# Performance work log

Hardware: AMD Instinct MI355X
Metric: run time of the kernel (lower is better)

Reference implementation:

```python
import jax, jax.numpy as jnp
import numpy as np
import math

B, S, D_MODEL, H = 128, 256, 128, 8
D_K = D_MODEL // H
FACTOR = 5
SAMPLE_K = FACTOR * int(math.ceil(math.log(S)))   # 30 sampled keys per query
N_TOP = min(FACTOR * int(math.ceil(math.log(S))), S)  # 30 active queries
KSIZE = 7


def setup_inputs() -> dict:
    key = jax.random.key(0)
    ks = jax.random.split(key, 10)
    s = 0.05
    return {
        "query": jax.random.normal(ks[0], (B, S, D_MODEL), jnp.float32),
        "key": jax.random.normal(ks[1], (B, S, D_MODEL), jnp.float32),
        "value": jax.random.normal(ks[2], (B, S, D_MODEL), jnp.float32),
        "conv_k_w": jax.random.normal(ks[3], (S, S, KSIZE), jnp.float32) * s,
        "conv_k_b": jax.random.normal(ks[4], (S,), jnp.float32) * s,
        "conv_v_w": jax.random.normal(ks[5], (S, S, KSIZE), jnp.float32) * s,
        "conv_v_b": jax.random.normal(ks[6], (S,), jnp.float32) * s,
        "lin_w": jax.random.normal(ks[7], (D_MODEL, D_MODEL), jnp.float32) * s,
        "lin_b": jax.random.normal(ks[8], (D_MODEL,), jnp.float32) * s,
        "index_sample": jax.random.randint(ks[9], (S, SAMPLE_K), 0, S),
    }


def _rotary(x):
    # x: [B,S,D]; complex rotation of consecutive pairs, angle = pos * theta^{-2i/D}
    half = D_MODEL // 2
    freqs = 1.0 / (10000.0 ** (jnp.arange(0, D_MODEL, 2, dtype=jnp.float32) / D_MODEL))
    ang = jnp.arange(S, dtype=jnp.float32)[:, None] * freqs[None, :]  # [S, half]
    cos, sin = jnp.cos(ang), jnp.sin(ang)
    xr = x.reshape(B, S, half, 2)
    out_r = xr[..., 0] * cos - xr[..., 1] * sin
    out_i = xr[..., 0] * sin + xr[..., 1] * cos
    return jnp.stack([out_r, out_i], axis=-1).reshape(B, S, D_MODEL)


def _causal_conv(x, w, b):
    # x: [B, C=S, L=D_MODEL]; causal => left-pad (KSIZE-1). w: [C_out, C_in, K]
    y = jax.lax.conv_general_dilated(
        x, w, window_strides=(1,), padding=[(KSIZE - 1, 0)],
        dimension_numbers=("NCH", "OIH", "NCH"))
    return y + b[None, :, None]


def reference(query, key, value, conv_k_w, conv_k_b, conv_v_w, conv_v_b,
              lin_w, lin_b, index_sample):
    q, k = _rotary(query), _rotary(key)
    k = _causal_conv(k, conv_k_w, conv_k_b)        # conv over seq-as-channels
    v = _causal_conv(value, conv_v_w, conv_v_b)
    # [B,S,D] -> [B,H,S,Dk]
    q = q.reshape(B, S, H, D_K).transpose(0, 2, 1, 3)
    k = k.reshape(B, S, H, D_K).transpose(0, 2, 1, 3)
    v = v.reshape(B, S, H, D_K).transpose(0, 2, 1, 3)

    # --- ProbSparse attention (Informer), mask=None ---
    k_sample = k[:, :, index_sample, :]                       # [B,H,S,SAMPLE_K,Dk]
    qk_sample = jnp.einsum('bhld,bhlsd->bhls', q, k_sample)   # sampled scores
    M = qk_sample.max(axis=-1) - qk_sample.mean(axis=-1)      # sparsity measure [B,H,S]
    _, m_top = jax.lax.top_k(M, N_TOP)                        # active queries [B,H,u]
    q_reduce = jnp.take_along_axis(q, m_top[..., None], axis=2)  # [B,H,u,Dk]
    scores = jnp.einsum('bhud,bhld->bhul', q_reduce, k) / jnp.sqrt(jnp.float32(D_K))
    attn = jax.nn.softmax(scores, axis=-1)
    out_top = jnp.einsum('bhul,bhld->bhud', attn, v)          # [B,H,u,Dk]
    # initial context = mean of V (no mask); overwrite rows of active queries
    context = jnp.broadcast_to(v.mean(axis=2, keepdims=True), (B, H, S, D_K))
    bi = jnp.arange(B)[:, None, None]
    hi = jnp.arange(H)[None, :, None]
    context = context.at[bi, hi, m_top].set(out_top)

    x = context.transpose(0, 2, 1, 3).reshape(B, S, D_MODEL)
    return x @ lin_w.T + lin_b
```

## Files before the change

### kernel.cpp

```cpp
#include <hip/hip_runtime.h>
#include <math.h>

constexpr int B_  = 128;
constexpr int S_  = 256;
constexpr int D_  = 128;
constexpr int H_  = 8;
constexpr int DK_ = 16;
constexpr int SK_ = 30;
constexpr int NT_ = 30;

typedef short short8  __attribute__((ext_vector_type(8)));
typedef float floatx4 __attribute__((ext_vector_type(4)));

__device__ inline ushort bf16_rne(float f) {
    unsigned u = __float_as_uint(f);
    u += 0x7fffu + ((u >> 16) & 1u);
    return (ushort)(u >> 16);
}
__device__ inline float bf16_to_f(ushort h) {
    return __uint_as_float(((unsigned)h) << 16);
}

__global__ __launch_bounds__(256) void wprep_kernel(
    const float* __restrict__ wk, const float* __restrict__ wv,
    const float* __restrict__ lw,
    ushort* __restrict__ wk_hi, ushort* __restrict__ wk_lo,
    ushort* __restrict__ wv_hi,
    ushort* __restrict__ lw_hi, ushort* __restrict__ lw_lo)
{
    int tid = blockIdx.x * 256 + threadIdx.x;
    if (tid < 131072) {
        int which = tid >> 16;
        int oi = tid & 65535;
        const float* src = (which ? wv : wk) + (size_t)oi * 7;
#pragma unroll
        for (int t = 0; t < 7; t++) {
            float f = src[t];
            ushort hi = bf16_rne(f);
            size_t dst = (size_t)t * 65536 + oi;
            if (which) {
                wv_hi[dst] = hi;
            } else {
                wk_hi[dst] = hi;
                wk_lo[dst] = bf16_rne(f - bf16_to_f(hi));
            }
        }
    } else {
        int ec = tid - 131072;
        float f = lw[ec];
        ushort hi = bf16_rne(f);
        lw_hi[ec] = hi;
        lw_lo[ec] = bf16_rne(f - bf16_to_f(hi));
    }
}

__global__ __launch_bounds__(256) void trig_kernel(float* __restrict__ tab)
{
    int tid = blockIdx.x * 256 + threadIdx.x;
    int f = tid & 63, l = tid >> 6;
    double freq = exp(((double)(-f) / 64.0) * 9.210340371976184);
    double ang  = (double)l * freq;
    tab[tid * 2]     = (float)cos(ang);
    tab[tid * 2 + 1] = (float)sin(ang);
}

__global__ __launch_bounds__(256) void rotary_kernel(
    const float* __restrict__ q, const float* __restrict__ k,
    const float* __restrict__ tab,
    float* __restrict__ q_h, float* __restrict__ k_rot)
{
    int tid = blockIdx.x * 256 + threadIdx.x;
    int f = tid & 63;
    int l = (tid >> 6) & 255;
    int b = tid >> 14;

    float2 cs = *(const float2*)(tab + (size_t)(l * 64 + f) * 2);
    float c = cs.x, s = cs.y;

    int base = (b * S_ + l) * D_ + 2 * f;
    float q0 = q[base], q1 = q[base + 1];
    float k0 = k[base], k1 = k[base + 1];

    float qr = q0 * c - q1 * s;
    float qi = q0 * s + q1 * c;
    float kr = k0 * c - k1 * s;
    float ki = k0 * s + k1 * c;

    k_rot[base]     = kr;
    k_rot[base + 1] = ki;

    int d = 2 * f;
    int h = d >> 4, dk = d & 15;
    int qb = ((b * H_ + h) * S_ + l) * DK_ + dk;
    q_h[qb]     = qr;
    q_h[qb + 1] = qi;
}

__global__ __launch_bounds__(256) void transcvt_kernel(
    const float* __restrict__ k_rot, const float* __restrict__ value,
    ushort* __restrict__ khi_t, ushort* __restrict__ klo_t,
    ushort* __restrict__ vhi_t)
{
    __shared__ float tile[64 * 132];
    int b = blockIdx.x;
    int which = blockIdx.y;
    int tid = threadIdx.x;
    const float* src = which ? value : k_rot;

    for (int lc = 0; lc < 4; lc++) {
        __syncthreads();
        for (int s = tid; s < 2048; s += 256) {
            int l = s >> 5, c4 = s & 31;
            *(float4*)(tile + l * 132 + c4 * 4) =
                *(const float4*)(src + (((size_t)b * 256) + lc * 64 + l) * 128 + c4 * 4);
        }
        __syncthreads();
        int d = tid >> 1, half = tid & 1;
        alignas(16) ushort hh[32], ll[32];
#pragma unroll
        for (int j = 0; j < 32; j++) {
            float f = tile[(half * 32 + j) * 132 + d];
            ushort hb = bf16_rne(f);
            hh[j] = hb;
            ll[j] = bf16_rne(f - bf16_to_f(hb));
        }
        size_t off = (((size_t)b * 128) + d) * 256 + lc * 64 + half * 32;
        if (which) {
#pragma unroll
            for (int m = 0; m < 4; m++) ((uint4*)(vhi_t + off))[m] = ((uint4*)hh)[m];
        } else {
#pragma unroll
            for (int m = 0; m < 4; m++) ((uint4*)(khi_t + off))[m] = ((uint4*)hh)[m];
#pragma unroll
            for (int m = 0; m < 4; m++) ((uint4*)(klo_t + off))[m] = ((uint4*)ll)[m];
        }
    }
}

__global__ __launch_bounds__(256, 4) void conv3_kernel(
    const ushort* __restrict__ khi_t, const ushort* __restrict__ klo_t,
    const ushort* __restrict__ vhi_t,
    const ushort* __restrict__ wk_hi, const ushort* __restrict__ wk_lo,
    const ushort* __restrict__ wv_hi,
    const float* __restrict__ kbias, const float* __restrict__ vbias,
    float* __restrict__ k_h, float* __restrict__ v_h)
{
    constexpr int LI = 72;
    __shared__ ushort xhi[134 * LI];
    __shared__ ushort xlo[134 * LI];

    const bool kp = (blockIdx.z == 0);
    const ushort* xhi_g = kp ? khi_t : vhi_t;
    const ushort* whi   = kp ? wk_hi : wv_hi;
    const float*  bias  = kp ? kbias : vbias;
    float* yh           = kp ? k_h : v_h;

    int b    = blockIdx.x;
    int oblk = blockIdx.y * 64;
    int tid  = threadIdx.x;
    int lane = tid & 63, wid = tid >> 6;
    int lm = lane & 15, kb = lane >> 4;
    int ow = wid >> 1, dw = wid & 1;
    int obase = oblk + ow * 32;
    int dbase = dw * 64;

    floatx4 acc[8];
#pragma unroll
    for (int i = 0; i < 8; i++) acc[i] = (floatx4){0.f, 0.f, 0.f, 0.f};

    for (int idx = tid; idx < 6 * LI; idx += 256) { xhi[idx] = 0; xlo[idx] = 0; }

    const ushort* abase_h = xhi + (dbase + lm) * LI + kb * 8;
    const ushort* abase_l = xlo + (dbase + lm) * LI + kb * 8;

    for (int ic = 0; ic < 4; ic++) {
        __syncthreads();
        for (int s = tid; s < 1024; s += 256) {
            int d = s >> 3, p = s & 7;
            size_t g = (((size_t)b * 128) + d) * 256 + ic * 64 + p * 8;
            *(short8*)(xhi + (d + 6) * LI + p * 8) = *(const short8*)(xhi_g + g);
            if (kp)
                *(short8*)(xlo + (d + 6) * LI + p * 8) = *(const short8*)(klo_t + g);
        }
        __syncthreads();
#pragma unroll
        for (int ks2 = 0; ks2 < 2; ks2++) {
            int ibase = ic * 64 + ks2 * 32 + kb * 8;
#pragma unroll
            for (int t = 0; t < 7; t++) {
                short8 xh[4], xl[4];
#pragma unroll
                for (int nd = 0; nd < 4; nd++) {
                    xh[nd] = *(const short8*)(abase_h + (nd * 16 + t) * LI + ks2 * 32);
                    if (kp) xl[nd] = *(const short8*)(abase_l + (nd * 16 + t) * LI + ks2 * 32);
                }
                short8 wh[2], wl[2];
#pragma unroll
                for (int po = 0; po < 2; po++) {
                    size_t woff = (size_t)t * 65536 + (size_t)(obase + po * 16 + lm) * 256 + ibase;
                    wh[po] = *(const short8*)(whi + woff);
                    if (kp) wl[po] = *(const short8*)(wk_lo + woff);
                }
#pragma unroll
                for (int po = 0; po < 2; po++) {
#pragma unroll
                    for (int nd = 0; nd < 4; nd++) {
                        int a = po * 4 + nd;
                        acc[a] = __builtin_amdgcn_mfma_f32_16x16x32_bf16(xh[nd], wh[po], acc[a], 0, 0, 0);
                        if (kp) {
                            acc[a] = __builtin_amdgcn_mfma_f32_16x16x32_bf16(xl[nd], wh[po], acc[a], 0, 0, 0);
                            acc[a] = __builtin_amdgcn_mfma_f32_16x16x32_bf16(xh[nd], wl[po], acc[a], 0, 0, 0);
                        }
                    }
                }
            }
        }
    }

#pragma unroll
    for (int po = 0; po < 2; po++) {
        int o = obase + po * 16 + lm;
        float bv = bias[o];
#pragma unroll
        for (int nd = 0; nd < 4; nd++) {
            int dhi = dw * 4 + nd;
#pragma unroll
            for (int r = 0; r < 4; r++) {
                int dk = kb * 4 + r;
                yh[(((size_t)b * 8 + dhi) * 256 + o) * 16 + dk] = acc[po * 4 + nd][r] + bv;
            }
        }
    }
}

__global__ __launch_bounds__(256) void topk_kernel(
    const float* __restrict__ q_h, const float* __restrict__ k_h,
    const int* __restrict__ idxs, int* __restrict__ sel)
{
    __shared__ float ks[S_ * 20];
    __shared__ float Marr[S_];
    __shared__ int cnt;
    int bh  = blockIdx.x;
    int tid = threadIdx.x;
    if (tid == 0) cnt = 0;

    const float* kp = k_h + (size_t)bh * S_ * DK_;
    for (int idx = tid; idx < S_ * DK_; idx += 256)
        ks[(idx >> 4) * 20 + (idx & 15)] = kp[idx];
    __syncthreads();

    float qr[16];
    const float4* qp = (const float4*)(q_h + ((size_t)bh * S_ + tid) * DK_);
#pragma unroll
    for (int i = 0; i < 4; i++) {
        float4 t4 = qp[i];
        qr[4*i] = t4.x; qr[4*i+1] = t4.y; qr[4*i+2] = t4.z; qr[4*i+3] = t4.w;
    }
    int idxr[SK_];
    const int* ip = idxs + tid * SK_;
#pragma unroll
    for (int s = 0; s < SK_; s++) idxr[s] = ip[s];

    float mx = -1e30f, sm = 0.f;
#pragma unroll
    for (int s = 0; s < SK_; s++) {
        const float4* kr = (const float4*)(ks + idxr[s] * 20);
        float4 k0 = kr[0], k1 = kr[1], k2 = kr[2], k3 = kr[3];
        float d0 = qr[0]*k0.x, d1 = qr[1]*k0.y, d2 = qr[2]*k0.z, d3 = qr[3]*k0.w;
        d0 = fmaf(qr[4],  k1.x, d0); d1 = fmaf(qr[5],  k1.y, d1);
        d2 = fmaf(qr[6],  k1.z, d2); d3 = fmaf(qr[7],  k1.w, d3);
        d0 = fmaf(qr[8],  k2.x, d0); d1 = fmaf(qr[9],  k2.y, d1);
        d2 = fmaf(qr[10], k2.z, d2); d3 = fmaf(qr[11], k2.w, d3);
        d0 = fmaf(qr[12], k3.x, d0); d1 = fmaf(qr[13], k3.y, d1);
        d2 = fmaf(qr[14], k3.z, d2); d3 = fmaf(qr[15], k3.w, d3);
        float dot = (d0 + d1) + (d2 + d3);
        mx = fmaxf(mx, dot);
        sm += dot;
    }
    float M = mx - sm * (1.0f / 30.0f);
    Marr[tid] = M;
    __syncthreads();

    int higher = 0;
    for (int j = 0; j < S_; j++) {
        float Mj = Marr[j];
        if (Mj > M || (Mj == M && j < tid)) higher++;
    }
    if (higher < NT_) {
        int slot = atomicAdd(&cnt, 1);
        sel[bh * NT_ + slot] = tid;
    }
}

__global__ __launch_bounds__(256) void attn_kernel(
    const float* __restrict__ q_h, const float* __restrict__ k_h,
    const float* __restrict__ v_h, const int* __restrict__ sel,
    ushort* __restrict__ ctx_hi, ushort* __restrict__ ctx_lo)
{
    __shared__ float ks[S_ * 20];
    __shared__ float vs[S_ * 20];
    __shared__ float P[NT_][S_ + 1];
    __shared__ float qs[NT_][16];
    __shared__ float partial[16][17];
    __shared__ float vmean_s[16];
    __shared__ int sel_s[NT_];
    __shared__ int selflag[S_];

    int bh = blockIdx.x, b = bh >> 3, h = bh & 7;
    int tid = threadIdx.x;

    const float* kp = k_h + (size_t)bh * S_ * DK_;
    const float* vp = v_h + (size_t)bh * S_ * DK_;
    for (int idx = tid; idx < S_ * DK_; idx += 256) {
        int r = idx >> 4, c = idx & 15;
        ks[r * 20 + c] = kp[idx];
        vs[r * 20 + c] = vp[idx];
    }
    selflag[tid] = 0;
    if (tid < NT_) sel_s[tid] = sel[bh * NT_ + tid];
    __syncthreads();
    if (tid < NT_) selflag[sel_s[tid]] = 1;
    for (int idx = tid; idx < NT_ * 16; idx += 256) {
        int u = idx >> 4, c = idx & 15;
        qs[u][c] = q_h[((size_t)bh * S_ + sel_s[u]) * DK_ + c];
    }
    {
        int dk = tid & 15, chunk = tid >> 4;
        float s = 0.f;
#pragma unroll
        for (int r = 0; r < 16; r++) s += vs[(chunk * 16 + r) * 20 + dk];
        partial[chunk][dk] = s;
    }
    __syncthreads();
    if (tid < 16) {
        float s = 0.f;
#pragma unroll
        for (int c = 0; c < 16; c++) s += partial[c][tid];
        vmean_s[tid] = s * (1.0f / 256.0f);
    }
    __syncthreads();

    if (!selflag[tid]) {
        alignas(16) ushort hh[16], ll[16];
#pragma unroll
        for (int i = 0; i < 16; i++) {
            float v = vmean_s[i];
            ushort hb = bf16_rne(v);
            hh[i] = hb;
            ll[i] = bf16_rne(v - bf16_to_f(hb));
        }
        size_t off = ((size_t)(b * S_ + tid)) * D_ + h * DK_;
        ((uint4*)(ctx_hi + off))[0] = ((uint4*)hh)[0];
        ((uint4*)(ctx_hi + off))[1] = ((uint4*)hh)[1];
        ((uint4*)(ctx_lo + off))[0] = ((uint4*)ll)[0];
        ((uint4*)(ctx_lo + off))[1] = ((uint4*)ll)[1];
    }

    int g = tid >> 3, j = tid & 7;
    if (g < NT_) {
        float qreg[16];
        const float4* q4 = (const float4*)qs[g];
#pragma unroll
        for (int i = 0; i < 4; i++) {
            float4 t4 = q4[i];
            qreg[4*i] = t4.x; qreg[4*i+1] = t4.y; qreg[4*i+2] = t4.z; qreg[4*i+3] = t4.w;
        }
        float sc[32];
        float mx = -1e30f;
#pragma unroll
        for (int li = 0; li < 32; li++) {
            int l = j + li * 8;
            const float4* kr = (const float4*)(ks + l * 20);
            float4 k0 = kr[0], k1 = kr[1], k2 = kr[2], k3 = kr[3];
            float d0 = qreg[0]*k0.x, d1 = qreg[1]*k0.y, d2 = qreg[2]*k0.z, d3 = qreg[3]*k0.w;
            d0 = fmaf(qreg[4],  k1.x, d0); d1 = fmaf(qreg[5],  k1.y, d1);
            d2 = fmaf(qreg[6],  k1.z, d2); d3 = fmaf(qreg[7],  k1.w, d3);
            d0 = fmaf(qreg[8],  k2.x, d0); d1 = fmaf(qreg[9],  k2.y, d1);
            d2 = fmaf(qreg[10], k2.z, d2); d3 = fmaf(qreg[11], k2.w, d3);
            d0 = fmaf(qreg[12], k3.x, d0); d1 = fmaf(qreg[13], k3.y, d1);
            d2 = fmaf(qreg[14], k3.z, d2); d3 = fmaf(qreg[15], k3.w, d3);
            sc[li] = ((d0 + d1) + (d2 + d3)) * 0.25f;
            mx = fmaxf(mx, sc[li]);
        }
        mx = fmaxf(mx, __shfl_xor(mx, 1));
        mx = fmaxf(mx, __shfl_xor(mx, 2));
        mx = fmaxf(mx, __shfl_xor(mx, 4));
        float se = 0.f;
#pragma unroll
        for (int li = 0; li < 32; li++) {
            float e = __expf(sc[li] - mx);
            P[g][j + li * 8] = e;
            se += e;
        }
        se += __shfl_xor(se, 1);
        se += __shfl_xor(se, 2);
        se += __shfl_xor(se, 4);
        float inv = 1.0f / se;

        int dk0 = j * 2;
        float o0 = 0.f, o1 = 0.f;
#pragma unroll 8
        for (int l = 0; l < S_; l++) {
            float p = P[g][l];
            float2 vv = *(const float2*)(vs + l * 20 + dk0);
            o0 = fmaf(p, vv.x, o0);
            o1 = fmaf(p, vv.y, o1);
        }
        int lrow = sel_s[g];
        float v0 = o0 * inv, v1 = o1 * inv;
        ushort h0 = bf16_rne(v0), h1 = bf16_rne(v1);
        ushort l0 = bf16_rne(v0 - bf16_to_f(h0));
        ushort l1 = bf16_rne(v1 - bf16_to_f(h1));
        size_t off = ((size_t)(b * S_ + lrow)) * D_ + h * DK_ + dk0;
        *(uint*)(ctx_hi + off) = (uint)h0 | ((uint)h1 << 16);
        *(uint*)(ctx_lo + off) = (uint)l0 | ((uint)l1 << 16);
    }
}

__global__ __launch_bounds__(256) void linear_mfma_kernel(
    const ushort* __restrict__ ctx_hi, const ushort* __restrict__ ctx_lo,
    const ushort* __restrict__ w_hi, const ushort* __restrict__ w_lo,
    const float* __restrict__ bias, float* __restrict__ out)
{
    __shared__ ushort ahi[128 * 136];
    __shared__ ushort alo[128 * 136];

    int tid  = threadIdx.x;
    int lane = tid & 63, wid = tid >> 6;
    int lm = lane & 15, kb = lane >> 4;
    size_t rowbase = (size_t)blockIdx.x * 128;

    for (int idx = tid; idx < 2048; idx += 256) {
        int row = idx >> 4, c16 = idx & 15;
        short8 vh = *(const short8*)(ctx_hi + (rowbase + row) * 128 + c16 * 8);
        short8 vl = *(const short8*)(ctx_lo + (rowbase + row) * 128 + c16 * 8);
        *(short8*)(ahi + row * 136 + c16 * 8) = vh;
        *(short8*)(alo + row * 136 + c16 * 8) = vl;
    }
    __syncthreads();

    floatx4 acc[16];
#pragma unroll
    for (int i = 0; i < 16; i++) acc[i] = (floatx4){0.f, 0.f, 0.f, 0.f};

    const ushort* arow_h = ahi + (wid * 32 + lm) * 136 + kb * 8;
    const ushort* arow_l = alo + (wid * 32 + lm) * 136 + kb * 8;

#pragma unroll
    for (int kstep = 0; kstep < 4; kstep++) {
        short8 afh[2], afl[2];
#pragma unroll
        for (int mf = 0; mf < 2; mf++) {
            afh[mf] = *(const short8*)(arow_h + mf * 16 * 136 + kstep * 32);
            afl[mf] = *(const short8*)(arow_l + mf * 16 * 136 + kstep * 32);
        }
        short8 bfh[8], bfl[8];
#pragma unroll
        for (int nf = 0; nf < 8; nf++) {
            bfh[nf] = *(const short8*)(w_hi + (size_t)(nf * 16 + lm) * 128 + kstep * 32 + kb * 8);
            bfl[nf] = *(const short8*)(w_lo + (size_t)(nf * 16 + lm) * 128 + kstep * 32 + kb * 8);
        }
#pragma unroll
        for (int mf = 0; mf < 2; mf++) {
#pragma unroll
            for (int nf = 0; nf < 8; nf++) {
                int a = mf * 8 + nf;
                acc[a] = __builtin_amdgcn_mfma_f32_16x16x32_bf16(afh[mf], bfh[nf], acc[a], 0, 0, 0);
                acc[a] = __builtin_amdgcn_mfma_f32_16x16x32_bf16(afl[mf], bfh[nf], acc[a], 0, 0, 0);
                acc[a] = __builtin_amdgcn_mfma_f32_16x16x32_bf16(afh[mf], bfl[nf], acc[a], 0, 0, 0);
            }
        }
    }

#pragma unroll
    for (int nf = 0; nf < 8; nf++) {
        int col = nf * 16 + lm;
        float bv = bias[col];
#pragma unroll
        for (int mf = 0; mf < 2; mf++) {
#pragma unroll
            for (int r = 0; r < 4; r++) {
                int row = wid * 32 + mf * 16 + kb * 4 + r;
                out[(rowbase + row) * 128 + col] = acc[mf * 8 + nf][r] + bv;
            }
        }
    }
}

extern "C" void kernel_launch(void* const* d_in, const int* in_sizes, int n_in,
                              void* d_out, int out_size, void* d_ws, size_t ws_size,
                              hipStream_t stream)
{
    const float* query = (const float*)d_in[0];
    const float* key   = (const float*)d_in[1];
    const float* value = (const float*)d_in[2];
    const float* ckw   = (const float*)d_in[3];
    const float* ckb   = (const float*)d_in[4];
    const float* cvw   = (const float*)d_in[5];
    const float* cvb   = (const float*)d_in[6];
    const float* lw    = (const float*)d_in[7];
    const float* lb    = (const float*)d_in[8];
    const int*   isamp = (const int*)d_in[9];
    float* out = (float*)d_out;
    float* ws  = (float*)d_ws;

    const size_t NBSD = (size_t)B_ * S_ * D_;
    float* q_h  = ws;
    float* kbuf = ws + NBSD;
    float* k_h  = ws + 2 * NBSD;
    float* v_h  = ws + 3 * NBSD;
    int*   sel  = (int*)(ws + 4 * NBSD);
    ushort* wk_hi = (ushort*)(sel + B_ * H_ * NT_);
    ushort* wk_lo = wk_hi + 7 * 65536;
    ushort* wv_hi = wk_lo + 7 * 65536;
    ushort* lw_hi = wv_hi + 7 * 65536;
    ushort* lw_lo = lw_hi + 16384;
    float*  trig  = (float*)(lw_lo + 16384);
    ushort* khi_t = (ushort*)(trig + 32768);
    ushort* klo_t = khi_t + NBSD;
    ushort* vhi_t = klo_t + NBSD;
    ushort* ctx_hi = (ushort*)kbuf;
    ushort* ctx_lo = ctx_hi + NBSD;

    wprep_kernel<<<dim3(576), 256, 0, stream>>>(ckw, cvw, lw, wk_hi, wk_lo, wv_hi, lw_hi, lw_lo);
    trig_kernel<<<dim3(64), 256, 0, stream>>>(trig);
    rotary_kernel<<<dim3((B_ * S_ * 64) / 256), 256, 0, stream>>>(query, key, trig, q_h, kbuf);
    transcvt_kernel<<<dim3(B_, 2), 256, 0, stream>>>(kbuf, value, khi_t, klo_t, vhi_t);
    conv3_kernel<<<dim3(B_, 4, 2), 256, 0, stream>>>(khi_t, klo_t, vhi_t,
                                                     wk_hi, wk_lo, wv_hi,
                                                     ckb, cvb, k_h, v_h);
    topk_kernel<<<dim3(B_ * H_), 256, 0, stream>>>(q_h, k_h, isamp, sel);
    attn_kernel<<<dim3(B_ * H_), 256, 0, stream>>>(q_h, k_h, v_h, sel, ctx_hi, ctx_lo);
    linear_mfma_kernel<<<dim3(256), 256, 0, stream>>>(ctx_hi, ctx_lo, lw_hi, lw_lo, lb, out);
}
```

Baseline: 284.5 us.

## Fuse trig, rotary, transpose-convert and topk+attention kernels; retile conv warps

Trig-table generation moves into the weight-prep kernel. Rotary, bf16 split and transpose are merged into one kernel so the rotated key is no longer round-tripped through global memory. Top-k selection and attention become one kernel, which removes the sel buffer and a second load of K. The probability matrix in shared memory is replaced by register broadcast via shuffles. The conv warp tiling changes from a 2x2 split to four output-row tiles per warp over 32 d-columns, trading fewer A-operand reads for more weight loads.

```diff
diff --git a/kernel.cpp b/kernel.cpp
--- a/kernel.cpp
+++ b/kernel.cpp
@@ -26,7 +26,8 @@
     const float* __restrict__ lw,
     ushort* __restrict__ wk_hi, ushort* __restrict__ wk_lo,
     ushort* __restrict__ wv_hi,
-    ushort* __restrict__ lw_hi, ushort* __restrict__ lw_lo)
+    ushort* __restrict__ lw_hi, ushort* __restrict__ lw_lo,
+    float* __restrict__ trig)
 {
     int tid = blockIdx.x * 256 + threadIdx.x;
     if (tid < 131072) {
@@ -45,76 +46,61 @@
                 wk_lo[dst] = bf16_rne(f - bf16_to_f(hi));
             }
         }
-    } else {
+    } else if (tid < 147456) {
         int ec = tid - 131072;
         float f = lw[ec];
         ushort hi = bf16_rne(f);
         lw_hi[ec] = hi;
         lw_lo[ec] = bf16_rne(f - bf16_to_f(hi));
-    }
-}
-
-__global__ __launch_bounds__(256) void trig_kernel(float* __restrict__ tab)
-{
-    int tid = blockIdx.x * 256 + threadIdx.x;
-    int f = tid & 63, l = tid >> 6;
-    double freq = exp(((double)(-f) / 64.0) * 9.210340371976184);
-    double ang  = (double)l * freq;
-    tab[tid * 2]     = (float)cos(ang);
-    tab[tid * 2 + 1] = (float)sin(ang);
-}
-
-__global__ __launch_bounds__(256) void rotary_kernel(
+    } else {
+        int t2 = tid - 147456;
+        int f = t2 & 63, l = t2 >> 6;
+        double freq = exp(((double)(-f) / 64.0) * 9.210340371976184);
+        double ang  = (double)l * freq;
+        trig[t2 * 2]     = (float)cos(ang);
+        trig[t2 * 2 + 1] = (float)sin(ang);
+    }
+}
+
+__global__ __launch_bounds__(256) void rotcvt_kernel(
     const float* __restrict__ q, const float* __restrict__ k,
-    const float* __restrict__ tab,
-    float* __restrict__ q_h, float* __restrict__ k_rot)
-{
-    int tid = blockIdx.x * 256 + threadIdx.x;
-    int f = tid & 63;
-    int l = (tid >> 6) & 255;
-    int b = tid >> 14;
-
-    float2 cs = *(const float2*)(tab + (size_t)(l * 64 + f) * 2);
-    float c = cs.x, s = cs.y;
-
-    int base = (b * S_ + l) * D_ + 2 * f;
-    float q0 = q[base], q1 = q[base + 1];
-    float k0 = k[base], k1 = k[base + 1];
-
-    float qr = q0 * c - q1 * s;
-    float qi = q0 * s + q1 * c;
-    float kr = k0 * c - k1 * s;
-    float ki = k0 * s + k1 * c;
-
-    k_rot[base]     = kr;
-    k_rot[base + 1] = ki;
-
-    int d = 2 * f;
-    int h = d >> 4, dk = d & 15;
-    int qb = ((b * H_ + h) * S_ + l) * DK_ + dk;
-    q_h[qb]     = qr;
-    q_h[qb + 1] = qi;
-}
-
-__global__ __launch_bounds__(256) void transcvt_kernel(
-    const float* __restrict__ k_rot, const float* __restrict__ value,
+    const float* __restrict__ value, const float* __restrict__ trig,
+    float* __restrict__ q_h,
     ushort* __restrict__ khi_t, ushort* __restrict__ klo_t,
     ushort* __restrict__ vhi_t)
 {
     __shared__ float tile[64 * 132];
-    int b = blockIdx.x;
-    int which = blockIdx.y;
+    int b  = blockIdx.x;
+    int lc = blockIdx.y;
     int tid = threadIdx.x;
-    const float* src = which ? value : k_rot;
-
-    for (int lc = 0; lc < 4; lc++) {
-        __syncthreads();
-        for (int s = tid; s < 2048; s += 256) {
-            int l = s >> 5, c4 = s & 31;
-            *(float4*)(tile + l * 132 + c4 * 4) =
-                *(const float4*)(src + (((size_t)b * 256) + lc * 64 + l) * 128 + c4 * 4);
-        }
-        __syncthreads();
+
+    for (int s = tid; s < 2048; s += 256) {
+        int l = s >> 5, c4 = s & 31;
+        int lg = lc * 64 + l;
+        float4 qv = *(const float4*)(q + (((size_t)b * 256) + lg) * 128 + c4 * 4);
+        float4 tg = *(const float4*)(trig + ((size_t)lg * 64 + 2 * c4) * 2);
+        float r0 = qv.x * tg.x - qv.y * tg.y;
+        float i0 = qv.x * tg.y + qv.y * tg.x;
+        float r1 = qv.z * tg.z - qv.w * tg.w;
+        float i1 = qv.z * tg.w + qv.w * tg.z;
+        int h = c4 >> 2, dk = (c4 & 3) * 4;
+        *(float4*)(q_h + (((size_t)b * 8 + h) * 256 + lg) * 16 + dk) =
+            make_float4(r0, i0, r1, i1);
+    }
+
+    for (int s = tid; s < 2048; s += 256) {
+        int l = s >> 5, c4 = s & 31;
+        int lg = lc * 64 + l;
+        float4 kv = *(const float4*)(k + (((size_t)b * 256) + lg) * 128 + c4 * 4);
+        float4 tg = *(const float4*)(trig + ((size_t)lg * 64 + 2 * c4) * 2);
+        float r0 = kv.x * tg.x - kv.y * tg.y;
+        float i0 = kv.x * tg.y + kv.y * tg.x;
+        float r1 = kv.z * tg.z - kv.w * tg.w;
+        float i1 = kv.z * tg.w + kv.w * tg.z;
+        *(float4*)(tile + l * 132 + c4 * 4) = make_float4(r0, i0, r1, i1);
+    }
+    __syncthreads();
+    {
         int d = tid >> 1, half = tid & 1;
         alignas(16) ushort hh[32], ll[32];
 #pragma unroll
@@ -125,19 +111,32 @@
             ll[j] = bf16_rne(f - bf16_to_f(hb));
         }
         size_t off = (((size_t)b * 128) + d) * 256 + lc * 64 + half * 32;
-        if (which) {
-#pragma unroll
-            for (int m = 0; m < 4; m++) ((uint4*)(vhi_t + off))[m] = ((uint4*)hh)[m];
-        } else {
-#pragma unroll
-            for (int m = 0; m < 4; m++) ((uint4*)(khi_t + off))[m] = ((uint4*)hh)[m];
-#pragma unroll
-            for (int m = 0; m < 4; m++) ((uint4*)(klo_t + off))[m] = ((uint4*)ll)[m];
-        }
-    }
-}
-
-__global__ __launch_bounds__(256, 4) void conv3_kernel(
+#pragma unroll
+        for (int m = 0; m < 4; m++) ((uint4*)(khi_t + off))[m] = ((uint4*)hh)[m];
+#pragma unroll
+        for (int m = 0; m < 4; m++) ((uint4*)(klo_t + off))[m] = ((uint4*)ll)[m];
+    }
+    __syncthreads();
+
+    for (int s = tid; s < 2048; s += 256) {
+        int l = s >> 5, c4 = s & 31;
+        *(float4*)(tile + l * 132 + c4 * 4) =
+            *(const float4*)(value + (((size_t)b * 256) + lc * 64 + l) * 128 + c4 * 4);
+    }
+    __syncthreads();
+    {
+        int d = tid >> 1, half = tid & 1;
+        alignas(16) ushort hh[32];
+#pragma unroll
+        for (int j = 0; j < 32; j++)
+            hh[j] = bf16_rne(tile[(half * 32 + j) * 132 + d]);
+        size_t off = (((size_t)b * 128) + d) * 256 + lc * 64 + half * 32;
+#pragma unroll
+        for (int m = 0; m < 4; m++) ((uint4*)(vhi_t + off))[m] = ((uint4*)hh)[m];
+    }
+}
+
+__global__ __launch_bounds__(256, 4) void conv4_kernel(
     const ushort* __restrict__ khi_t, const ushort* __restrict__ klo_t,
     const ushort* __restrict__ vhi_t,
     const ushort* __restrict__ wk_hi, const ushort* __restrict__ wk_lo,
@@ -155,14 +154,12 @@
     const float*  bias  = kp ? kbias : vbias;
     float* yh           = kp ? k_h : v_h;
 
-    int b    = blockIdx.x;
-    int oblk = blockIdx.y * 64;
-    int tid  = threadIdx.x;
-    int lane = tid & 63, wid = tid >> 6;
+    int b     = blockIdx.x;
+    int obase = blockIdx.y * 64;
+    int tid   = threadIdx.x;
+    int lane  = tid & 63, dw = tid >> 6;
     int lm = lane & 15, kb = lane >> 4;
-    int ow = wid >> 1, dw = wid & 1;
-    int obase = oblk + ow * 32;
-    int dbase = dw * 64;
+    int dbase = dw * 32;
 
     floatx4 acc[8];
 #pragma unroll
@@ -188,24 +185,24 @@
             int ibase = ic * 64 + ks2 * 32 + kb * 8;
 #pragma unroll
             for (int t = 0; t < 7; t++) {
-                short8 xh[4], xl[4];
-#pragma unroll
-                for (int nd = 0; nd < 4; nd++) {
+                short8 xh[2], xl[2];
+#pragma unroll
+                for (int nd = 0; nd < 2; nd++) {
                     xh[nd] = *(const short8*)(abase_h + (nd * 16 + t) * LI + ks2 * 32);
                     if (kp) xl[nd] = *(const short8*)(abase_l + (nd * 16 + t) * LI + ks2 * 32);
                 }
-                short8 wh[2], wl[2];
-#pragma unroll
-                for (int po = 0; po < 2; po++) {
+                short8 wh[4], wl[4];
+#pragma unroll
+                for (int po = 0; po < 4; po++) {
                     size_t woff = (size_t)t * 65536 + (size_t)(obase + po * 16 + lm) * 256 + ibase;
                     wh[po] = *(const short8*)(whi + woff);
                     if (kp) wl[po] = *(const short8*)(wk_lo + woff);
                 }
 #pragma unroll
-                for (int po = 0; po < 2; po++) {
-#pragma unroll
-                    for (int nd = 0; nd < 4; nd++) {
-                        int a = po * 4 + nd;
+                for (int po = 0; po < 4; po++) {
+#pragma unroll
+                    for (int nd = 0; nd < 2; nd++) {
+                        int a = po * 2 + nd;
                         acc[a] = __builtin_amdgcn_mfma_f32_16x16x32_bf16(xh[nd], wh[po], acc[a], 0, 0, 0);
                         if (kp) {
                             acc[a] = __builtin_amdgcn_mfma_f32_16x16x32_bf16(xl[nd], wh[po], acc[a], 0, 0, 0);
@@ -218,36 +215,48 @@
     }
 
 #pragma unroll
-    for (int po = 0; po < 2; po++) {
+    for (int po = 0; po < 4; po++) {
         int o = obase + po * 16 + lm;
         float bv = bias[o];
 #pragma unroll
-        for (int nd = 0; nd < 4; nd++) {
-            int dhi = dw * 4 + nd;
+        for (int nd = 0; nd < 2; nd++) {
+            int dhi = dw * 2 + nd;
 #pragma unroll
             for (int r = 0; r < 4; r++) {
                 int dk = kb * 4 + r;
-                yh[(((size_t)b * 8 + dhi) * 256 + o) * 16 + dk] = acc[po * 4 + nd][r] + bv;
+                yh[(((size_t)b * 8 + dhi) * 256 + o) * 16 + dk] = acc[po * 2 + nd][r] + bv;
             }
         }
     }
 }
 
-__global__ __launch_bounds__(256) void topk_kernel(
+__global__ __launch_bounds__(256) void topk_attn_kernel(
     const float* __restrict__ q_h, const float* __restrict__ k_h,
-    const int* __restrict__ idxs, int* __restrict__ sel)
+    const float* __restrict__ v_h, const int* __restrict__ idxs,
+    ushort* __restrict__ ctx_hi, ushort* __restrict__ ctx_lo)
 {
     __shared__ float ks[S_ * 20];
+    __shared__ float vs[S_ * 20];
     __shared__ float Marr[S_];
+    __shared__ float qs[NT_][16];
+    __shared__ float partial[16][17];
+    __shared__ float vmean_s[16];
+    __shared__ int sel_s[NT_];
+    __shared__ int selflag[S_];
     __shared__ int cnt;
-    int bh  = blockIdx.x;
+
+    int bh = blockIdx.x, b = bh >> 3, h = bh & 7;
     int tid = threadIdx.x;
     if (tid == 0) cnt = 0;
+    selflag[tid] = 0;
 
     const float* kp = k_h + (size_t)bh * S_ * DK_;
-    for (int idx = tid; idx < S_ * DK_; idx += 256)
-        ks[(idx >> 4) * 20 + (idx & 15)] = kp[idx];
-    __syncthreads();
+    const float* vp = v_h + (size_t)bh * S_ * DK_;
+    for (int idx = tid; idx < S_ * DK_; idx += 256) {
+        int r = idx >> 4, c = idx & 15;
+        ks[r * 20 + c] = kp[idx];
+        vs[r * 20 + c] = vp[idx];
+    }
 
     float qr[16];
     const float4* qp = (const float4*)(q_h + ((size_t)bh * S_ + tid) * DK_);
@@ -260,6 +269,7 @@
     const int* ip = idxs + tid * SK_;
 #pragma unroll
     for (int s = 0; s < SK_; s++) idxr[s] = ip[s];
+    __syncthreads();
 
     float mx = -1e30f, sm = 0.f;
 #pragma unroll
@@ -277,66 +287,41 @@
         mx = fmaxf(mx, dot);
         sm += dot;
     }
-    float M = mx - sm * (1.0f / 30.0f);
-    Marr[tid] = M;
-    __syncthreads();
-
-    int higher = 0;
-    for (int j = 0; j < S_; j++) {
-        float Mj = Marr[j];
-        if (Mj > M || (Mj == M && j < tid)) higher++;
-    }
-    if (higher < NT_) {
-        int slot = atomicAdd(&cnt, 1);
-        sel[bh * NT_ + slot] = tid;
-    }
-}
-
-__global__ __launch_bounds__(256) void attn_kernel(
-    const float* __restrict__ q_h, const float* __restrict__ k_h,
-    const float* __restrict__ v_h, const int* __restrict__ sel,
-    ushort* __restrict__ ctx_hi, ushort* __restrict__ ctx_lo)
-{
-    __shared__ float ks[S_ * 20];
-    __shared__ float vs[S_ * 20];
-    __shared__ float P[NT_][S_ + 1];
-    __shared__ float qs[NT_][16];
-    __shared__ float partial[16][17];
-    __shared__ float vmean_s[16];
-    __shared__ int sel_s[NT_];
-    __shared__ int selflag[S_];
-
-    int bh = blockIdx.x, b = bh >> 3, h = bh & 7;
-    int tid = threadIdx.x;
-
-    const float* kp = k_h + (size_t)bh * S_ * DK_;
-    const float* vp = v_h + (size_t)bh * S_ * DK_;
-    for (int idx = tid; idx < S_ * DK_; idx += 256) {
-        int r = idx >> 4, c = idx & 15;
-        ks[r * 20 + c] = kp[idx];
-        vs[r * 20 + c] = vp[idx];
-    }
-    selflag[tid] = 0;
-    if (tid < NT_) sel_s[tid] = sel[bh * NT_ + tid];
-    __syncthreads();
-    if (tid < NT_) selflag[sel_s[tid]] = 1;
+    Marr[tid] = mx - sm * (1.0f / 30.0f);
+
+    {
+        int dk = tid & 15, chunk = tid >> 4;
+        float s = 0.f;
+#pragma unroll
+        for (int r = 0; r < 16; r++) s += vs[(chunk * 16 + r) * 20 + dk];
+        partial[chunk][dk] = s;
+    }
+    __syncthreads();
+
+    if (tid < 16) {
+        float s = 0.f;
+#pragma unroll
+        for (int c = 0; c < 16; c++) s += partial[c][tid];
+        vmean_s[tid] = s * (1.0f / 256.0f);
+    }
+    {
+        float M = Marr[tid];
+        int higher = 0;
+        for (int j = 0; j < S_; j++) {
+            float Mj = Marr[j];
+            if (Mj > M || (Mj == M && j < tid)) higher++;
+        }
+        if (higher < NT_) {
+            int slot = atomicAdd(&cnt, 1);
+            sel_s[slot] = tid;
+            selflag[tid] = 1;
+        }
+    }
+    __syncthreads();
+
     for (int idx = tid; idx < NT_ * 16; idx += 256) {
         int u = idx >> 4, c = idx & 15;
         qs[u][c] = q_h[((size_t)bh * S_ + sel_s[u]) * DK_ + c];
-    }
-    {
-        int dk = tid & 15, chunk = tid >> 4;
-        float s = 0.f;
-#pragma unroll
-        for (int r = 0; r < 16; r++) s += vs[(chunk * 16 + r) * 20 + dk];
-        partial[chunk][dk] = s;
-    }
-    __syncthreads();
-    if (tid < 16) {
-        float s = 0.f;
-#pragma unroll
-        for (int c = 0; c < 16; c++) s += partial[c][tid];
-        vmean_s[tid] = s * (1.0f / 256.0f);
     }
     __syncthreads();
 
@@ -365,8 +350,8 @@
             float4 t4 = q4[i];
             qreg[4*i] = t4.x; qreg[4*i+1] = t4.y; qreg[4*i+2] = t4.z; qreg[4*i+3] = t4.w;
         }
-        float sc[32];
-        float mx = -1e30f;
+        float e[32];
+        float mxs = -1e30f;
 #pragma unroll
         for (int li = 0; li < 32; li++) {
             int l = j + li * 8;
@@ -379,18 +364,17 @@
             d2 = fmaf(qreg[10], k2.z, d2); d3 = fmaf(qreg[11], k2.w, d3);
             d0 = fmaf(qreg[12], k3.x, d0); d1 = fmaf(qreg[13], k3.y, d1);
             d2 = fmaf(qreg[14], k3.z, d2); d3 = fmaf(qreg[15], k3.w, d3);
-            sc[li] = ((d0 + d1) + (d2 + d3)) * 0.25f;
-            mx = fmaxf(mx, sc[li]);
-        }
-        mx = fmaxf(mx, __shfl_xor(mx, 1));
-        mx = fmaxf(mx, __shfl_xor(mx, 2));
-        mx = fmaxf(mx, __shfl_xor(mx, 4));
+            e[li] = ((d0 + d1) + (d2 + d3)) * 0.25f;
+            mxs = fmaxf(mxs, e[li]);
+        }
+        mxs = fmaxf(mxs, __shfl_xor(mxs, 1));
+        mxs = fmaxf(mxs, __shfl_xor(mxs, 2));
+        mxs = fmaxf(mxs, __shfl_xor(mxs, 4));
         float se = 0.f;
 #pragma unroll
         for (int li = 0; li < 32; li++) {
-            float e = __expf(sc[li] - mx);
-            P[g][j + li * 8] = e;
-            se += e;
+            e[li] = __expf(e[li] - mxs);
+            se += e[li];
         }
         se += __shfl_xor(se, 1);
         se += __shfl_xor(se, 2);
@@ -398,13 +382,16 @@
         float inv = 1.0f / se;
 
         int dk0 = j * 2;
+        int gbase = tid & 56;
         float o0 = 0.f, o1 = 0.f;
-#pragma unroll 8
-        for (int l = 0; l < S_; l++) {
-            float p = P[g][l];
-            float2 vv = *(const float2*)(vs + l * 20 + dk0);
-            o0 = fmaf(p, vv.x, o0);
-            o1 = fmaf(p, vv.y, o1);
+        for (int li = 0; li < 32; li++) {
+#pragma unroll
+            for (int m = 0; m < 8; m++) {
+                float p = __shfl(e[li], gbase | m);
+                float2 vv = *(const float2*)(vs + (li * 8 + m) * 20 + dk0);
+                o0 = fmaf(p, vv.x, o0);
+                o1 = fmaf(p, vv.y, o1);
+            }
         }
         int lrow = sel_s[g];
         float v0 = o0 * inv, v1 = o1 * inv;
@@ -522,14 +509,15 @@
     ushort* ctx_hi = (ushort*)kbuf;
     ushort* ctx_lo = ctx_hi + NBSD;
 
-    wprep_kernel<<<dim3(576), 256, 0, stream>>>(ckw, cvw, lw, wk_hi, wk_lo, wv_hi, lw_hi, lw_lo);
-    trig_kernel<<<dim3(64), 256, 0, stream>>>(trig);
-    rotary_kernel<<<dim3((B_ * S_ * 64) / 256), 256, 0, stream>>>(query, key, trig, q_h, kbuf);
-    transcvt_kernel<<<dim3(B_, 2), 256, 0, stream>>>(kbuf, value, khi_t, klo_t, vhi_t);
-    conv3_kernel<<<dim3(B_, 4, 2), 256, 0, stream>>>(khi_t, klo_t, vhi_t,
+    wprep_kernel<<<dim3(640), 256, 0, stream>>>(ckw, cvw, lw, wk_hi, wk_lo,
+                                                wv_hi, lw_hi, lw_lo, trig);
+    rotcvt_kernel<<<dim3(B_, 4), 256, 0, stream>>>(query, key, value, trig,
+                                                   q_h, khi_t, klo_t, vhi_t);
+    conv4_kernel<<<dim3(B_, 4, 2), 256, 0, stream>>>(khi_t, klo_t, vhi_t,
                                                      wk_hi, wk_lo, wv_hi,
                                                      ckb, cvb, k_h, v_h);
-    topk_kernel<<<dim3(B_ * H_), 256, 0, stream>>>(q_h, k_h, isamp, sel);
-    attn_kernel<<<dim3(B_ * H_), 256, 0, stream>>>(q_h, k_h, v_h, sel, ctx_hi, ctx_lo);
-    linear_mfma_kernel<<<dim3(256), 256, 0, stream>>>(ctx_hi, ctx_lo, lw_hi, lw_lo, lb, out);
-}
+    topk_attn_kernel<<<dim3(B_ * H_), 256, 0, stream>>>(q_h, k_h, v_h, isamp,
+                                                        ctx_hi, ctx_lo);
+    linear_mfma_kernel<<<dim3(256), 256, 0, stream>>>(ctx_hi, ctx_lo, lw_hi,
+                                                      lw_lo, lb, out);
+}
```

Measured after the change: 350.2 us. 1.23x slower.
